# Optimization experiments

Measured on AMD Instinct MI355X. Metric: run time of the kernel, lower is better.

## Reference

```python
import jax, jax.numpy as jnp
import numpy as np

B, T, C = 32, 128, 64
E, H = 8, 4            # feat_dim, num_heads
D = E // H             # head_dim = 2
HID = 32               # hidden_dim


def setup_inputs() -> dict:
    key = jax.random.key(0)
    ks = jax.random.split(key, 20)
    s = 0.1
    return {
        "x": jax.random.normal(ks[0], (B, T, C), jnp.float32),
        # input_proj: Linear(C, C)
        "W_in": jax.random.normal(ks[1], (C, C), jnp.float32) * s,
        "b_in": jax.random.normal(ks[2], (C,), jnp.float32) * s,
        # time_step_score: Linear(C, C//4) -> GELU -> Linear(C//4, 1) -> Sigmoid
        "W_ts1": jax.random.normal(ks[3], (C // 4, C), jnp.float32) * s,
        "b_ts1": jax.random.normal(ks[4], (C // 4,), jnp.float32) * s,
        "W_ts2": jax.random.normal(ks[5], (1, C // 4), jnp.float32) * s,
        "b_ts2": jax.random.normal(ks[6], (1,), jnp.float32) * s,
        # per-channel GRU(1 -> E): torch gate order (r, z, n)
        "W_ih": jax.random.normal(ks[7], (C, 3 * E), jnp.float32) * s,      # input size 1
        "W_hh": jax.random.normal(ks[8], (C, 3 * E, E), jnp.float32) * s,
        "b_ih": jax.random.normal(ks[9], (C, 3 * E), jnp.float32) * s,
        "b_hh": jax.random.normal(ks[10], (C, 3 * E), jnp.float32) * s,
        # shared MultiheadAttention(E, 4): packed in_proj + out_proj
        "W_qkv": jax.random.normal(ks[11], (3 * E, E), jnp.float32) * s,
        "b_qkv": jax.random.normal(ks[12], (3 * E,), jnp.float32) * s,
        "W_o": jax.random.normal(ks[13], (E, E), jnp.float32) * s,
        "b_o": jax.random.normal(ks[14], (E,), jnp.float32) * s,
        # out_proj: Linear(C*E, HID)
        "W_out": jax.random.normal(ks[15], (HID, C * E), jnp.float32) * s,
        "b_out": jax.random.normal(ks[16], (HID,), jnp.float32) * s,
    }


def _forward(x, W_in, b_in, W_ts1, b_ts1, W_ts2, b_ts2,
             W_ih, W_hh, b_ih, b_hh, W_qkv, b_qkv, W_o, b_o, W_out, b_out):
    bs, ts, c = x.shape
    # time step importance: per-timestep MLP over the raw features
    h1 = jax.nn.gelu(jnp.einsum('btc,fc->btf', x, W_ts1) + b_ts1, approximate=False)
    ts_imp = jax.nn.sigmoid(jnp.einsum('btf,of->bto', h1, W_ts2) + b_ts2)[..., 0]  # [B,T]

    xp = jnp.einsum('btc,dc->btd', x, W_in) + b_in  # [B,T,C]

    # Batched per-channel GRU scan over time. state h: [B,C,E]
    def step(h, x_t):
        gi = x_t[:, :, None] * W_ih[None] + b_ih          # [B,C,3E]
        gh = jnp.einsum('bce,cge->bcg', h, W_hh) + b_hh   # [B,C,3E]
        ir, iz, inn = gi[..., :E], gi[..., E:2 * E], gi[..., 2 * E:]
        hr, hz, hn = gh[..., :E], gh[..., E:2 * E], gh[..., 2 * E:]
        r = jax.nn.sigmoid(ir + hr)
        z = jax.nn.sigmoid(iz + hz)
        n = jnp.tanh(inn + r * hn)
        h_new = (1.0 - z) * n + z * h
        return h_new, h_new

    h0 = jnp.zeros((bs, c, E), xp.dtype)
    _, hs = jax.lax.scan(step, h0, jnp.transpose(xp, (1, 0, 2)))  # [T,B,C,E]
    hs_bcte = jnp.transpose(hs, (1, 2, 0, 3))                     # [B,C,T,E]

    # Shared MHA applied independently per channel (batched over B*C)
    qkv = jnp.einsum('bcte,fe->bctf', hs_bcte, W_qkv) + b_qkv     # [B,C,T,3E]
    q, k, v = qkv[..., :E], qkv[..., E:2 * E], qkv[..., 2 * E:]
    def heads(t):
        return t.reshape(bs, c, ts, H, D)
    q, k, v = heads(q), heads(k), heads(v)
    scores = jnp.einsum('bcthd,bcshd->bchts', q, k) / np.sqrt(D)
    attn = jax.nn.softmax(scores, axis=-1)
    o = jnp.einsum('bchts,bcshd->bcthd', attn, v).reshape(bs, c, ts, E)
    attn_out = jnp.einsum('bcte,fe->bctf', o, W_o) + b_o          # [B,C,T,E]
    attention = jnp.transpose(attn_out, (0, 2, 1, 3))             # [B,T,C,E]

    out_flat = jnp.transpose(hs, (1, 0, 2, 3)).reshape(bs, ts, c * E)  # [B,T,C*E]
    out = jnp.einsum('btf,hf->bth', out_flat, W_out) + b_out           # [B,T,HID]

    feat_imp = jax.nn.sigmoid(attention.sum(axis=(1, 3)))   # [B,C]
    tsf_imp = jax.nn.sigmoid(attention.sum(axis=-1))        # [B,T,C]
    return out[:, -1, :], feat_imp, ts_imp, tsf_imp


def reference(x, W_in, b_in, W_ts1, b_ts1, W_ts2, b_ts2,
              W_ih, W_hh, b_ih, b_hh, W_qkv, b_qkv, W_o, b_o, W_out, b_out):
    return _forward(x, W_in, b_in, W_ts1, b_ts1, W_ts2, b_ts2,
                    W_ih, W_hh, b_ih, b_hh, W_qkv, b_qkv, W_o, b_o, W_out, b_out)
```

## Files before the change

### kernel.cpp

```cpp
#include <hip/hip_runtime.h>
#include <hip/hip_bf16.h>
#include <math.h>

#define B_ 32
#define T_ 128
#define C_ 64
#define E_ 8
#define HID_ 32

__device__ __forceinline__ float sigmoidf_(float x) { return 1.0f / (1.0f + __expf(-x)); }
__device__ __forceinline__ float tanhf_(float x) {
    float xc = fminf(fmaxf(x, -15.0f), 15.0f);
    float e = __expf(2.0f * xc);
    return (e - 1.0f) / (e + 1.0f);
}

__global__ __launch_bounds__(64) void k_pre(
    const float* __restrict__ x, const float* __restrict__ W_in, const float* __restrict__ b_in,
    float* __restrict__ xp)
{
    const int bt = blockIdx.x;
    const int tid = threadIdx.x;
    __shared__ __align__(16) float4 xs4[16];
    if (tid < 16) xs4[tid] = ((const float4*)(x + bt * C_))[tid];
    __syncthreads();
    float a = b_in[tid];
    const float4* w4 = (const float4*)(W_in + tid * C_);
#pragma unroll
    for (int k4 = 0; k4 < 16; ++k4) {
        float4 xv = xs4[k4];
        float4 wv = w4[k4];
        a = fmaf(xv.x, wv.x, a); a = fmaf(xv.y, wv.y, a);
        a = fmaf(xv.z, wv.z, a); a = fmaf(xv.w, wv.w, a);
    }
    xp[bt * C_ + tid] = a;
}

__global__ __launch_bounds__(64) void k_gru(
    const float* __restrict__ xp, const float* __restrict__ W_ih, const float* __restrict__ W_hh,
    const float* __restrict__ b_ih, const float* __restrict__ b_hh,
    float* __restrict__ hs, float* __restrict__ fh)
{
    const int tid = threadIdx.x;
    const int ci = tid >> 3;
    const int e = tid & 7;
    const int chain = blockIdx.x * 8 + ci;
    const int b = chain >> 6;
    const int c = chain & 63;

    __shared__ float xc[8][T_ + 1];

    for (int tt = 0; tt < 16; ++tt) {
        const int t = e * 16 + tt;
        xc[ci][t] = xp[(b * T_ + t) * C_ + c];
    }
    __syncthreads();

    float wr[E_], wz[E_], wn[E_];
#pragma unroll
    for (int j = 0; j < E_; ++j) {
        wr[j] = W_hh[(c * 24 + 0 * E_ + e) * E_ + j];
        wz[j] = W_hh[(c * 24 + 1 * E_ + e) * E_ + j];
        wn[j] = W_hh[(c * 24 + 2 * E_ + e) * E_ + j];
    }
    const float wir = W_ih[c * 24 + e], wiz = W_ih[c * 24 + E_ + e], win = W_ih[c * 24 + 2 * E_ + e];
    const float bir = b_ih[c * 24 + e], biz = b_ih[c * 24 + E_ + e], bin_ = b_ih[c * 24 + 2 * E_ + e];
    const float bhr = b_hh[c * 24 + e], bhz = b_hh[c * 24 + E_ + e], bhn = b_hh[c * 24 + 2 * E_ + e];

    float h = 0.0f;
    float* ho = hs + (size_t)chain * T_ * E_ + e;
    for (int t = 0; t < T_; ++t) {
        float xv = xc[ci][t];
        float gr = fmaf(xv, wir, bir) + bhr;
        float gz = fmaf(xv, wiz, biz) + bhz;
        float gn = fmaf(xv, win, bin_);
        float hn = bhn;
#pragma unroll
        for (int j = 0; j < E_; ++j) {
            float hj = __shfl(h, j, E_);
            gr = fmaf(hj, wr[j], gr);
            gz = fmaf(hj, wz[j], gz);
            hn = fmaf(hj, wn[j], hn);
        }
        float r = sigmoidf_(gr);
        float z = sigmoidf_(gz);
        float nn = tanhf_(fmaf(r, hn, gn));
        h = (1.0f - z) * nn + z * h;
        ho[t * E_] = h;
    }
    fh[chain * E_ + e] = h;
}

__global__ __launch_bounds__(128) void k_attn(
    const float* __restrict__ hs, const float* __restrict__ W_qkv, const float* __restrict__ b_qkv,
    const float* __restrict__ W_o, const float* __restrict__ b_o,
    float* __restrict__ feat_imp, float* __restrict__ tsf_imp)
{
    const int bc = blockIdx.x;
    const int b = bc >> 6, c = bc & 63;
    const int t = threadIdx.x;

    __shared__ __align__(16) float ks[T_][E_];
    __shared__ __align__(16) float vs[T_][E_];
    __shared__ float red[T_];

    float hrow[E_];
    {
        const float4* hp = (const float4*)(hs + (size_t)bc * T_ * E_ + t * E_);
        float4 h0 = hp[0], h1 = hp[1];
        hrow[0] = h0.x; hrow[1] = h0.y; hrow[2] = h0.z; hrow[3] = h0.w;
        hrow[4] = h1.x; hrow[5] = h1.y; hrow[6] = h1.z; hrow[7] = h1.w;
    }

    const float qscale = 0.70710678118654752f * 1.44269504088896341f;
    float q[E_];
#pragma unroll
    for (int f = 0; f < E_; ++f) {
        float a = b_qkv[f];
#pragma unroll
        for (int j = 0; j < E_; ++j) a = fmaf(hrow[j], W_qkv[f * E_ + j], a);
        q[f] = a * qscale;
    }
#pragma unroll
    for (int f = 0; f < E_; ++f) {
        float a = b_qkv[E_ + f];
#pragma unroll
        for (int j = 0; j < E_; ++j) a = fmaf(hrow[j], W_qkv[(E_ + f) * E_ + j], a);
        ks[t][f] = a;
    }
#pragma unroll
    for (int f = 0; f < E_; ++f) {
        float a = b_qkv[2 * E_ + f];
#pragma unroll
        for (int j = 0; j < E_; ++j) a = fmaf(hrow[j], W_qkv[(2 * E_ + f) * E_ + j], a);
        vs[t][f] = a;
    }
    __syncthreads();

    float l[4] = {0.f, 0.f, 0.f, 0.f};
    float acc[E_] = {0.f, 0.f, 0.f, 0.f, 0.f, 0.f, 0.f, 0.f};
    for (int s = 0; s < T_; ++s) {
        float4 k0 = *(const float4*)&ks[s][0];
        float4 k1 = *(const float4*)&ks[s][4];
        float4 v0 = *(const float4*)&vs[s][0];
        float4 v1 = *(const float4*)&vs[s][4];
        float p0 = exp2f(fmaf(q[1], k0.y, q[0] * k0.x));
        float p1 = exp2f(fmaf(q[3], k0.w, q[2] * k0.z));
        float p2 = exp2f(fmaf(q[5], k1.y, q[4] * k1.x));
        float p3 = exp2f(fmaf(q[7], k1.w, q[6] * k1.z));
        l[0] += p0; l[1] += p1; l[2] += p2; l[3] += p3;
        acc[0] = fmaf(p0, v0.x, acc[0]); acc[1] = fmaf(p0, v0.y, acc[1]);
        acc[2] = fmaf(p1, v0.z, acc[2]); acc[3] = fmaf(p1, v0.w, acc[3]);
        acc[4] = fmaf(p2, v1.x, acc[4]); acc[5] = fmaf(p2, v1.y, acc[5]);
        acc[6] = fmaf(p3, v1.z, acc[6]); acc[7] = fmaf(p3, v1.w, acc[7]);
    }

    float S = 0.0f;
#pragma unroll
    for (int f = 0; f < E_; ++f) {
        float wsum = 0.0f;
#pragma unroll
        for (int fp = 0; fp < E_; ++fp) wsum += W_o[fp * E_ + f];
        S = fmaf(acc[f] / l[f >> 1], wsum, S);
    }
#pragma unroll
    for (int fp = 0; fp < E_; ++fp) S += b_o[fp];

    tsf_imp[(size_t)b * T_ * C_ + (size_t)t * C_ + c] = sigmoidf_(S);

    red[t] = S;
    __syncthreads();
    for (int off = 64; off > 0; off >>= 1) {
        if (t < off) red[t] += red[t + off];
        __syncthreads();
    }
    if (t == 0) feat_imp[bc] = sigmoidf_(red[0]);
}

__global__ __launch_bounds__(64) void k_ts(
    const float* __restrict__ x,
    const float* __restrict__ W_ts1, const float* __restrict__ b_ts1,
    const float* __restrict__ W_ts2, const float* __restrict__ b_ts2,
    float* __restrict__ ts_imp)
{
    const int bt = blockIdx.x;
    const int tid = threadIdx.x;
    __shared__ float xs[C_];
    __shared__ float h1[16];
    xs[tid] = x[bt * C_ + tid];
    __syncthreads();
    if (tid < 16) {
        float a = b_ts1[tid];
#pragma unroll
        for (int k = 0; k < C_; ++k) a = fmaf(xs[k], W_ts1[tid * C_ + k], a);
        h1[tid] = 0.5f * a * (1.0f + erff(a * 0.70710678118654752f));
    }
    __syncthreads();
    if (tid == 0) {
        float s = b_ts2[0];
#pragma unroll
        for (int k = 0; k < 16; ++k) s = fmaf(h1[k], W_ts2[k], s);
        ts_imp[bt] = sigmoidf_(s);
    }
}

__global__ __launch_bounds__(64) void k_out(
    const float* __restrict__ fh, const float* __restrict__ W_out, const float* __restrict__ b_out,
    float* __restrict__ out0)
{
    const int b = blockIdx.x;
    const int tid = threadIdx.x;
    __shared__ float hf[C_ * E_];
    const float4* src = (const float4*)(fh + (b * C_ + tid) * E_);
    float4* dst = (float4*)(hf + tid * E_);
    dst[0] = src[0];
    dst[1] = src[1];
    __syncthreads();
    if (tid < HID_) {
        float a = b_out[tid];
        const float* wo = W_out + tid * (C_ * E_);
        for (int k = 0; k < C_ * E_; ++k) a = fmaf(hf[k], wo[k], a);
        out0[b * HID_ + tid] = a;
    }
}

extern "C" void kernel_launch(void* const* d_in, const int* in_sizes, int n_in,
                              void* d_out, int out_size, void* d_ws, size_t ws_size,
                              hipStream_t stream) {
    (void)in_sizes; (void)n_in; (void)out_size; (void)ws_size;

    float* out0 = (float*)d_out;
    float* feat = out0 + B_ * HID_;
    float* tsim = feat + B_ * C_;
    float* tsf  = tsim + B_ * T_;

    const float* x     = (const float*)d_in[0];
    const float* W_in  = (const float*)d_in[1];
    const float* b_in  = (const float*)d_in[2];
    const float* W_ts1 = (const float*)d_in[3];
    const float* b_ts1 = (const float*)d_in[4];
    const float* W_ts2 = (const float*)d_in[5];
    const float* b_ts2 = (const float*)d_in[6];
    const float* W_ih  = (const float*)d_in[7];
    const float* W_hh  = (const float*)d_in[8];
    const float* b_ih  = (const float*)d_in[9];
    const float* b_hh  = (const float*)d_in[10];
    const float* W_qkv = (const float*)d_in[11];
    const float* b_qkv = (const float*)d_in[12];
    const float* W_o   = (const float*)d_in[13];
    const float* b_o   = (const float*)d_in[14];
    const float* W_out = (const float*)d_in[15];
    const float* b_out = (const float*)d_in[16];

    float* fhb = (float*)d_ws;
    float* xpb = fhb + B_ * C_ * E_;
    float* hsb = xpb + (size_t)B_ * T_ * C_;

    hipLaunchKernelGGL(k_pre, dim3(B_ * T_), dim3(64), 0, stream, x, W_in, b_in, xpb);
    hipLaunchKernelGGL(k_gru, dim3(B_ * C_ / 8), dim3(64), 0, stream,
                       xpb, W_ih, W_hh, b_ih, b_hh, hsb, fhb);
    hipLaunchKernelGGL(k_attn, dim3(B_ * C_), dim3(128), 0, stream,
                       hsb, W_qkv, b_qkv, W_o, b_o, feat, tsf);
    hipLaunchKernelGGL(k_ts, dim3(B_ * T_), dim3(64), 0, stream,
                       x, W_ts1, b_ts1, W_ts2, b_ts2, tsim);
    hipLaunchKernelGGL(k_out, dim3(B_), dim3(64), 0, stream,
                       fhb, W_out, b_out, out0);
}
```

Before: 103.9 us.

## Fuse input projection into GRU kernel and split attention keys across two thread halves

```diff
diff --git a/kernel.cpp b/kernel.cpp
--- a/kernel.cpp
+++ b/kernel.cpp
@@ -15,29 +15,9 @@
     return (e - 1.0f) / (e + 1.0f);
 }
 
-__global__ __launch_bounds__(64) void k_pre(
+__global__ __launch_bounds__(64) void k_gru(
     const float* __restrict__ x, const float* __restrict__ W_in, const float* __restrict__ b_in,
-    float* __restrict__ xp)
-{
-    const int bt = blockIdx.x;
-    const int tid = threadIdx.x;
-    __shared__ __align__(16) float4 xs4[16];
-    if (tid < 16) xs4[tid] = ((const float4*)(x + bt * C_))[tid];
-    __syncthreads();
-    float a = b_in[tid];
-    const float4* w4 = (const float4*)(W_in + tid * C_);
-#pragma unroll
-    for (int k4 = 0; k4 < 16; ++k4) {
-        float4 xv = xs4[k4];
-        float4 wv = w4[k4];
-        a = fmaf(xv.x, wv.x, a); a = fmaf(xv.y, wv.y, a);
-        a = fmaf(xv.z, wv.z, a); a = fmaf(xv.w, wv.w, a);
-    }
-    xp[bt * C_ + tid] = a;
-}
-
-__global__ __launch_bounds__(64) void k_gru(
-    const float* __restrict__ xp, const float* __restrict__ W_ih, const float* __restrict__ W_hh,
+    const float* __restrict__ W_ih, const float* __restrict__ W_hh,
     const float* __restrict__ b_ih, const float* __restrict__ b_hh,
     float* __restrict__ hs, float* __restrict__ fh)
 {
@@ -48,11 +28,32 @@
     const int b = chain >> 6;
     const int c = chain & 63;
 
+    __shared__ float wsh[8][C_];
     __shared__ float xc[8][T_ + 1];
 
+#pragma unroll
+    for (int i = 0; i < 8; ++i) {
+        int idx = tid * 8 + i;
+        int ci2 = idx >> 6;
+        int cc = (blockIdx.x * 8 + ci2) & 63;
+        wsh[ci2][idx & 63] = W_in[cc * C_ + (idx & 63)];
+    }
+    __syncthreads();
+
+    const float bi = b_in[c];
     for (int tt = 0; tt < 16; ++tt) {
         const int t = e * 16 + tt;
-        xc[ci][t] = xp[(b * T_ + t) * C_ + c];
+        const float4* xr = (const float4*)(x + (b * T_ + t) * C_);
+        float a = bi;
+#pragma unroll
+        for (int k4 = 0; k4 < 16; ++k4) {
+            float4 xv = xr[k4];
+            a = fmaf(xv.x, wsh[ci][k4 * 4 + 0], a);
+            a = fmaf(xv.y, wsh[ci][k4 * 4 + 1], a);
+            a = fmaf(xv.z, wsh[ci][k4 * 4 + 2], a);
+            a = fmaf(xv.w, wsh[ci][k4 * 4 + 3], a);
+        }
+        xc[ci][t] = a;
     }
     __syncthreads();
 
@@ -91,17 +92,22 @@
     fh[chain * E_ + e] = h;
 }
 
-__global__ __launch_bounds__(128) void k_attn(
+__global__ __launch_bounds__(256) void k_attn(
     const float* __restrict__ hs, const float* __restrict__ W_qkv, const float* __restrict__ b_qkv,
     const float* __restrict__ W_o, const float* __restrict__ b_o,
     float* __restrict__ feat_imp, float* __restrict__ tsf_imp)
 {
     const int bc = blockIdx.x;
     const int b = bc >> 6, c = bc & 63;
-    const int t = threadIdx.x;
+    const int tid = threadIdx.x;
+    const int t = tid & 127;
+    const int p = tid >> 7;
 
     __shared__ __align__(16) float ks[T_][E_];
     __shared__ __align__(16) float vs[T_][E_];
+    __shared__ __align__(16) float pacc[T_][12];
+    __shared__ float wssum[E_];
+    __shared__ float bsum_s;
     __shared__ float red[T_];
 
     float hrow[E_];
@@ -121,25 +127,41 @@
         for (int j = 0; j < E_; ++j) a = fmaf(hrow[j], W_qkv[f * E_ + j], a);
         q[f] = a * qscale;
     }
-#pragma unroll
-    for (int f = 0; f < E_; ++f) {
-        float a = b_qkv[E_ + f];
-#pragma unroll
-        for (int j = 0; j < E_; ++j) a = fmaf(hrow[j], W_qkv[(E_ + f) * E_ + j], a);
-        ks[t][f] = a;
-    }
-#pragma unroll
-    for (int f = 0; f < E_; ++f) {
-        float a = b_qkv[2 * E_ + f];
-#pragma unroll
-        for (int j = 0; j < E_; ++j) a = fmaf(hrow[j], W_qkv[(2 * E_ + f) * E_ + j], a);
-        vs[t][f] = a;
+    if (p == 0) {
+#pragma unroll
+        for (int f = 0; f < E_; ++f) {
+            float a = b_qkv[E_ + f];
+#pragma unroll
+            for (int j = 0; j < E_; ++j) a = fmaf(hrow[j], W_qkv[(E_ + f) * E_ + j], a);
+            ks[t][f] = a;
+        }
+    } else {
+#pragma unroll
+        for (int f = 0; f < E_; ++f) {
+            float a = b_qkv[2 * E_ + f];
+#pragma unroll
+            for (int j = 0; j < E_; ++j) a = fmaf(hrow[j], W_qkv[(2 * E_ + f) * E_ + j], a);
+            vs[t][f] = a;
+        }
+    }
+    if (tid < E_) {
+        float ws = 0.0f;
+#pragma unroll
+        for (int fp = 0; fp < E_; ++fp) ws += W_o[fp * E_ + tid];
+        wssum[tid] = ws;
+    }
+    if (tid == E_) {
+        float bs = 0.0f;
+#pragma unroll
+        for (int fp = 0; fp < E_; ++fp) bs += b_o[fp];
+        bsum_s = bs;
     }
     __syncthreads();
 
     float l[4] = {0.f, 0.f, 0.f, 0.f};
     float acc[E_] = {0.f, 0.f, 0.f, 0.f, 0.f, 0.f, 0.f, 0.f};
-    for (int s = 0; s < T_; ++s) {
+    const int s0 = p * 64;
+    for (int s = s0; s < s0 + 64; ++s) {
         float4 k0 = *(const float4*)&ks[s][0];
         float4 k1 = *(const float4*)&ks[s][4];
         float4 v0 = *(const float4*)&vs[s][0];
@@ -155,26 +177,31 @@
         acc[6] = fmaf(p3, v1.z, acc[6]); acc[7] = fmaf(p3, v1.w, acc[7]);
     }
 
-    float S = 0.0f;
-#pragma unroll
-    for (int f = 0; f < E_; ++f) {
-        float wsum = 0.0f;
-#pragma unroll
-        for (int fp = 0; fp < E_; ++fp) wsum += W_o[fp * E_ + f];
-        S = fmaf(acc[f] / l[f >> 1], wsum, S);
-    }
-#pragma unroll
-    for (int fp = 0; fp < E_; ++fp) S += b_o[fp];
-
-    tsf_imp[(size_t)b * T_ * C_ + (size_t)t * C_ + c] = sigmoidf_(S);
-
-    red[t] = S;
+    if (p == 1) {
+#pragma unroll
+        for (int i = 0; i < 4; ++i) pacc[t][i] = l[i];
+#pragma unroll
+        for (int j = 0; j < 8; ++j) pacc[t][4 + j] = acc[j];
+    }
+    __syncthreads();
+
+    if (p == 0) {
+#pragma unroll
+        for (int i = 0; i < 4; ++i) l[i] += pacc[t][i];
+#pragma unroll
+        for (int j = 0; j < 8; ++j) acc[j] += pacc[t][4 + j];
+        float S = bsum_s;
+#pragma unroll
+        for (int f = 0; f < E_; ++f) S = fmaf(acc[f] / l[f >> 1], wssum[f], S);
+        tsf_imp[(size_t)b * T_ * C_ + (size_t)t * C_ + c] = sigmoidf_(S);
+        red[t] = S;
+    }
     __syncthreads();
     for (int off = 64; off > 0; off >>= 1) {
-        if (t < off) red[t] += red[t + off];
+        if (p == 0 && t < off) red[t] += red[t + off];
         __syncthreads();
     }
-    if (t == 0) feat_imp[bc] = sigmoidf_(red[0]);
+    if (tid == 0) feat_imp[bc] = sigmoidf_(red[0]);
 }
 
 __global__ __launch_bounds__(64) void k_ts(
@@ -253,13 +280,11 @@
     const float* b_out = (const float*)d_in[16];
 
     float* fhb = (float*)d_ws;
-    float* xpb = fhb + B_ * C_ * E_;
-    float* hsb = xpb + (size_t)B_ * T_ * C_;
-
-    hipLaunchKernelGGL(k_pre, dim3(B_ * T_), dim3(64), 0, stream, x, W_in, b_in, xpb);
+    float* hsb = fhb + B_ * C_ * E_;
+
     hipLaunchKernelGGL(k_gru, dim3(B_ * C_ / 8), dim3(64), 0, stream,
-                       xpb, W_ih, W_hh, b_ih, b_hh, hsb, fhb);
-    hipLaunchKernelGGL(k_attn, dim3(B_ * C_), dim3(128), 0, stream,
+                       x, W_in, b_in, W_ih, W_hh, b_ih, b_hh, hsb, fhb);
+    hipLaunchKernelGGL(k_attn, dim3(B_ * C_), dim3(256), 0, stream,
                        hsb, W_qkv, b_qkv, W_o, b_o, feat, tsf);
     hipLaunchKernelGGL(k_ts, dim3(B_ * T_), dim3(64), 0, stream,
                        x, W_ts1, b_ts1, W_ts2, b_ts2, tsim);
```

After: 101.8 us. -2.1%, faster.
